# Performance work log

Measured on AMD Instinct MI355X. Metric: run time of the kernel, lower is better.

The kernel has to match this reference:

```python
import jax, jax.numpy as jnp
import numpy as np

GRID = 128          # fine voxel grid extent
N_PTS = 300000
C = 64              # hidden channels


def _encode(c, B):
    c = c.astype(np.int64)
    return (c[:, 0] * B + c[:, 1]) * B + c[:, 2]


def _kernel_map(in_coords, out_coords, offsets, n_out):
    """ME-style kernel map: for each kernel offset, (input_idx, output_idx) pairs
    where in_coord == out_coord + offset. Padded to a fixed length with a dummy
    output row n_out (sliced off later)."""
    B = GRID * 4
    keys = _encode(in_coords + 4, B)           # +4 shift keeps keys nonneg
    order = np.argsort(keys)
    skeys = keys[order]
    ins, outs = [], []
    for off in offsets:
        q = _encode(out_coords + 4 + off, B)
        pos = np.clip(np.searchsorted(skeys, q), 0, len(skeys) - 1)
        valid = skeys[pos] == q
        ins.append(order[pos[valid]].astype(np.int32))
        outs.append(np.nonzero(valid)[0].astype(np.int32))
    L = max(len(a) for a in ins)
    K = len(offsets)
    in_idx = np.zeros((K, L), np.int32)
    out_idx = np.full((K, L), n_out, np.int32)   # pad -> dummy row
    for k in range(K):
        m = len(ins[k])
        in_idx[k, :m] = ins[k]
        out_idx[k, :m] = outs[k]
    return in_idx, out_idx


def setup_inputs() -> dict:
    rng = np.random.default_rng(0)
    flat = rng.choice(GRID ** 3, size=N_PTS, replace=False)
    coords = np.stack(np.unravel_index(flat, (GRID,) * 3), axis=1).astype(np.int64)
    u = np.unique(coords // 2, axis=0)           # stride-2 output coords (coarse units)
    n2 = u.shape[0]

    r = np.arange(-1, 2)
    off27 = np.stack(np.meshgrid(r, r, r, indexing='ij'), -1).reshape(-1, 3)
    r2 = np.arange(0, 2)
    off8 = np.stack(np.meshgrid(r2, r2, r2, indexing='ij'), -1).reshape(-1, 3)

    map1_in, map1_out = _kernel_map(coords, coords, off27, N_PTS)   # k=3, s=1
    map2_in, map2_out = _kernel_map(coords, 2 * u, off8, n2)        # k=2, s=2
    map3_in, map3_out = _kernel_map(u, u, off27, n2)                # k=3, s=1 on coarse lattice

    key = jax.random.key(0)
    ks = jax.random.split(key, 8)
    sc1 = 1.0 / np.sqrt(27 * 8)
    sc2 = 1.0 / np.sqrt(8 * C)
    sc3 = 1.0 / np.sqrt(27 * C)
    return {
        'feats': jax.random.normal(ks[0], (N_PTS, 8), jnp.float32),
        'W1': jax.random.normal(ks[1], (27, 8, C), jnp.float32) * sc1,
        'b1': jax.random.normal(ks[2], (C,), jnp.float32) * 0.01,
        'W2': jax.random.normal(ks[3], (8, C, C), jnp.float32) * sc2,
        'b2': jax.random.normal(ks[4], (C,), jnp.float32) * 0.01,
        'W3': jax.random.normal(ks[5], (27, C, 8), jnp.float32) * sc3,
        'b3': jax.random.normal(ks[6], (8,), jnp.float32) * 0.01,
        'map1_in': jnp.asarray(map1_in), 'map1_out': jnp.asarray(map1_out),
        'map2_in': jnp.asarray(map2_in), 'map2_out': jnp.asarray(map2_out),
        'map3_in': jnp.asarray(map3_in), 'map3_out': jnp.asarray(map3_out),
        'n2': int(n2),
    }


def _sparse_conv(x, W, b, in_idx, out_idx, n_out):
    # gather-GEMM-scatter over K kernel offsets; padded pairs land on dummy row n_out
    y = jnp.zeros((n_out + 1, W.shape[-1]), x.dtype)
    for k in range(W.shape[0]):
        y = y.at[out_idx[k]].add(x[in_idx[k]] @ W[k])
    return y[:n_out] + b


def reference(feats, W1, b1, W2, b2, W3, b3,
              map1_in, map1_out, map2_in, map2_out, map3_in, map3_out, n2):
    n1 = feats.shape[0]
    h = jax.nn.relu(_sparse_conv(feats, W1, b1, map1_in, map1_out, n1))
    h = jax.nn.relu(_sparse_conv(h, W2, b2, map2_in, map2_out, n2))
    return _sparse_conv(h, W3, b3, map3_in, map3_out, n2)
```

## Files before the change

### kernel.cpp

```cpp
#include <hip/hip_runtime.h>


#define TPB 256

__device__ __forceinline__ int xcd_chunk(int bid, int nwg) {
  int q = nwg >> 3, r = nwg & 7;
  int xcd = bid & 7, idx = bid >> 3;
  int base = (xcd < r) ? xcd * (q + 1) : r * (q + 1) + (xcd - r) * q;
  return base + idx;
}

__global__ void __launch_bounds__(TPB)
k_build(const int* __restrict__ mi, const int* __restrict__ mo,
        int* __restrict__ tbl, int L, int n_out) {
  int k = blockIdx.y;
  int p = blockIdx.x * TPB + threadIdx.x;
  if (p >= L) return;
  int out = mo[(size_t)k * L + p];
  bool valid = out < n_out;
  if (__ballot(valid) == 0ull) return;
  if (valid) tbl[(size_t)k * n_out + out] = mi[(size_t)k * L + p];
}

__global__ void __launch_bounds__(TPB)
k_conv1(const float* __restrict__ x, const float* __restrict__ W1,
        const float* __restrict__ b1, const int* __restrict__ t1,
        float* __restrict__ h1, int n1) {
  int r = blockIdx.x * TPB + threadIdx.x;
  if (r >= n1) return;
  int j0 = blockIdx.y * 32;
  float acc[32];
#pragma unroll
  for (int j = 0; j < 32; ++j) acc[j] = 0.f;

  int icur = t1[r];
  const float4* xp = (const float4*)(x + (size_t)(icur >= 0 ? icur : 0) * 8);
  float4 ca = xp[0], cb = xp[1];
  bool vcur = icur >= 0;
#pragma unroll 1
  for (int k = 0; k < 27; ++k) {
    int inext = (k < 26) ? t1[(size_t)(k + 1) * n1 + r] : -1;
    const float4* np = (const float4*)(x + (size_t)(inext >= 0 ? inext : 0) * 8);
    float4 na = np[0], nb = np[1];
    if (!vcur) { ca = make_float4(0.f,0.f,0.f,0.f); cb = make_float4(0.f,0.f,0.f,0.f); }
    if (__ballot(vcur) != 0ull) {
      float xv[8] = {ca.x, ca.y, ca.z, ca.w, cb.x, cb.y, cb.z, cb.w};
      const float* __restrict__ Wk = W1 + (size_t)k * 512 + j0;
#pragma unroll
      for (int i = 0; i < 8; ++i)
#pragma unroll
        for (int j = 0; j < 32; ++j)
          acc[j] = fmaf(xv[i], Wk[i * 64 + j], acc[j]);
    }
    ca = na; cb = nb; vcur = inext >= 0;
  }
  float4* yr = (float4*)(h1 + (size_t)r * 64 + j0);
#pragma unroll
  for (int q = 0; q < 8; ++q) {
    float4 o;
    o.x = fmaxf(acc[4*q+0] + b1[j0+4*q+0], 0.f);
    o.y = fmaxf(acc[4*q+1] + b1[j0+4*q+1], 0.f);
    o.z = fmaxf(acc[4*q+2] + b1[j0+4*q+2], 0.f);
    o.w = fmaxf(acc[4*q+3] + b1[j0+4*q+3], 0.f);
    yr[q] = o;
  }
}

__global__ void __launch_bounds__(TPB)
k_conv2(const float* __restrict__ h1, const float* __restrict__ W2,
        const float* __restrict__ b2, const int* __restrict__ t2,
        float* __restrict__ h2, int n1, int n2, int nwg) {
  int b = xcd_chunk(blockIdx.x, nwg);
  int jq = b & 3, xb = b >> 2;
  int r = xb * TPB + threadIdx.x;
  if (r >= n2) return;
  int j0 = jq * 16;
  float acc[16];
#pragma unroll
  for (int j = 0; j < 16; ++j) acc[j] = 0.f;
  int idx = t2[r];
#pragma unroll 1
  for (int k = 0; k < 8; ++k) {
    int inext = (k < 7) ? t2[(size_t)(k + 1) * n2 + r] : 0;
    int row = idx >= 0 ? idx : n1;
    const float4* xr = (const float4*)(h1 + (size_t)row * 64);
    const float* __restrict__ Wk = W2 + (size_t)k * 4096 + j0;
#pragma unroll 4
    for (int c = 0; c < 16; ++c) {
      float4 xv = xr[c];
#pragma unroll
      for (int j = 0; j < 16; ++j) {
        acc[j] = fmaf(xv.x, Wk[(4*c+0)*64 + j], acc[j]);
        acc[j] = fmaf(xv.y, Wk[(4*c+1)*64 + j], acc[j]);
        acc[j] = fmaf(xv.z, Wk[(4*c+2)*64 + j], acc[j]);
        acc[j] = fmaf(xv.w, Wk[(4*c+3)*64 + j], acc[j]);
      }
    }
    idx = inext;
  }
  float4* yr = (float4*)(h2 + (size_t)r * 64 + j0);
#pragma unroll
  for (int q = 0; q < 4; ++q) {
    float4 o;
    o.x = fmaxf(acc[4*q+0] + b2[j0+4*q+0], 0.f);
    o.y = fmaxf(acc[4*q+1] + b2[j0+4*q+1], 0.f);
    o.z = fmaxf(acc[4*q+2] + b2[j0+4*q+2], 0.f);
    o.w = fmaxf(acc[4*q+3] + b2[j0+4*q+3], 0.f);
    yr[q] = o;
  }
}

__global__ void __launch_bounds__(TPB)
k_conv3(const float* __restrict__ h2, const float* __restrict__ W3,
        const float* __restrict__ b3, const int* __restrict__ t3,
        float* __restrict__ out, int n2, int nwg) {
  __shared__ float red[4][64][9];
  int b = xcd_chunk(blockIdx.x, nwg);
  int w = __builtin_amdgcn_readfirstlane(threadIdx.x >> 6);
  int l = threadIdx.x & 63;
  int r = b * 64 + l;
  int rc = r < n2 ? r : n2 - 1;
  float acc[8];
#pragma unroll
  for (int j = 0; j < 8; ++j) acc[j] = 0.f;
  int nk = (w < 3) ? 7 : 6;
  int idx = t3[(size_t)w * n2 + rc];
#pragma unroll 1
  for (int i = 0; i < nk; ++i) {
    int k = w + 4 * i;
    int row = idx >= 0 ? idx : n2;
    if (i + 1 < nk) idx = t3[(size_t)(k + 4) * n2 + rc];
    const float4* xr = (const float4*)(h2 + (size_t)row * 64);
    const float* __restrict__ Wk = W3 + (size_t)k * 512;
#pragma unroll
    for (int c = 0; c < 16; ++c) {
      float4 xv = xr[c];
      float hv[4] = {xv.x, xv.y, xv.z, xv.w};
#pragma unroll
      for (int u = 0; u < 4; ++u)
#pragma unroll
        for (int j = 0; j < 8; ++j)
          acc[j] = fmaf(hv[u], Wk[(4*c+u)*8 + j], acc[j]);
    }
  }
#pragma unroll
  for (int j = 0; j < 8; ++j) red[w][l][j] = acc[j];
  __syncthreads();
#pragma unroll
  for (int t = threadIdx.x; t < 512; t += TPB) {
    int row = t >> 3, ch = t & 7;
    int g = b * 64 + row;
    if (g < n2) {
      float s = red[0][row][ch] + red[1][row][ch]
              + red[2][row][ch] + red[3][row][ch];
      out[(size_t)g * 8 + ch] = s + b3[ch];
    }
  }
}

extern "C" void kernel_launch(void* const* d_in, const int* in_sizes, int n_in,
                              void* d_out, int out_size, void* d_ws, size_t ws_size,
                              hipStream_t stream) {
  const float* feats = (const float*)d_in[0];
  const float* W1 = (const float*)d_in[1];
  const float* b1 = (const float*)d_in[2];
  const float* W2 = (const float*)d_in[3];
  const float* b2 = (const float*)d_in[4];
  const float* W3 = (const float*)d_in[5];
  const float* b3 = (const float*)d_in[6];
  const int* m1i = (const int*)d_in[7];
  const int* m1o = (const int*)d_in[8];
  const int* m2i = (const int*)d_in[9];
  const int* m2o = (const int*)d_in[10];
  const int* m3i = (const int*)d_in[11];
  const int* m3o = (const int*)d_in[12];

  int n1 = in_sizes[0] / 8;
  int L1 = in_sizes[7] / 27;
  int L2 = in_sizes[9] / 8;
  int L3 = in_sizes[11] / 27;
  int n2 = out_size / 8;

  char* ws = (char*)d_ws;
  size_t y1_bytes = (size_t)(n1 + 1) * 64 * sizeof(float);
  size_t y2_bytes = (size_t)(n2 + 1) * 64 * sizeof(float);
  size_t t1_bytes = (size_t)27 * n1 * sizeof(int);
  size_t reg1_bytes = y2_bytes > t1_bytes ? y2_bytes : t1_bytes;
  float* y1 = (float*)ws;
  float* y2 = (float*)(ws + y1_bytes);
  int* t1 = (int*)(ws + y1_bytes);
  int* t2 = (int*)(ws + y1_bytes + reg1_bytes);
  int* t3 = (int*)(ws + y1_bytes + reg1_bytes + (size_t)8 * n2 * sizeof(int));

  hipMemsetAsync(t1, 0xFF, t1_bytes, stream);
  hipMemsetAsync(t2, 0xFF, (size_t)8 * n2 * sizeof(int), stream);
  hipMemsetAsync(t3, 0xFF, (size_t)27 * n2 * sizeof(int), stream);

  k_build<<<dim3((L1 + TPB - 1) / TPB, 27), TPB, 0, stream>>>(m1i, m1o, t1, L1, n1);
  k_build<<<dim3((L2 + TPB - 1) / TPB, 8), TPB, 0, stream>>>(m2i, m2o, t2, L2, n2);
  k_build<<<dim3((L3 + TPB - 1) / TPB, 27), TPB, 0, stream>>>(m3i, m3o, t3, L3, n2);

  k_conv1<<<dim3((n1 + TPB - 1) / TPB, 2), TPB, 0, stream>>>(feats, W1, b1, t1, y1, n1);

  hipMemsetAsync(y1 + (size_t)n1 * 64, 0, 64 * sizeof(float), stream);
  hipMemsetAsync(y2 + (size_t)n2 * 64, 0, 64 * sizeof(float), stream);

  int nb2 = ((n2 + TPB - 1) / TPB) * 4;
  k_conv2<<<nb2, TPB, 0, stream>>>(y1, W2, b2, t2, y2, n1, n2, nb2);

  int nb3 = (n2 + 63) / 64;
  k_conv3<<<nb3, TPB, 0, stream>>>(y2, W3, b3, t3, (float*)d_out, n2, nb3);
}
```

Baseline: 568.9 us.

## Coalesce conv1 stores via LDS staging, double rows per thread in conv3

conv1 now stages each block's 256x32 activated outputs in shared memory and writes them back as coalesced float4 rows. Before, each thread wrote its own strided 128-byte chunk. conv3 now processes two output rows per thread (128 rows per block), so each weight load is reused across two gathered inputs and half as many blocks are launched. The two index-table memsets are merged into one contiguous memset. The costs are extra LDS use and a barrier in conv1, plus more registers and fewer blocks in conv3.

```diff
diff --git a/kernel.cpp b/kernel.cpp
--- a/kernel.cpp
+++ b/kernel.cpp
@@ -26,20 +26,23 @@
 k_conv1(const float* __restrict__ x, const float* __restrict__ W1,
         const float* __restrict__ b1, const int* __restrict__ t1,
         float* __restrict__ h1, int n1) {
-  int r = blockIdx.x * TPB + threadIdx.x;
-  if (r >= n1) return;
+  __shared__ float st[256][33];
+  int tid = threadIdx.x;
+  int r0 = blockIdx.x * TPB;
+  int r = r0 + tid;
+  int rc = r < n1 ? r : n1 - 1;
   int j0 = blockIdx.y * 32;
   float acc[32];
 #pragma unroll
   for (int j = 0; j < 32; ++j) acc[j] = 0.f;
 
-  int icur = t1[r];
+  int icur = t1[rc];
   const float4* xp = (const float4*)(x + (size_t)(icur >= 0 ? icur : 0) * 8);
   float4 ca = xp[0], cb = xp[1];
   bool vcur = icur >= 0;
 #pragma unroll 1
   for (int k = 0; k < 27; ++k) {
-    int inext = (k < 26) ? t1[(size_t)(k + 1) * n1 + r] : -1;
+    int inext = (k < 26) ? t1[(size_t)(k + 1) * n1 + rc] : -1;
     const float4* np = (const float4*)(x + (size_t)(inext >= 0 ? inext : 0) * 8);
     float4 na = np[0], nb = np[1];
     if (!vcur) { ca = make_float4(0.f,0.f,0.f,0.f); cb = make_float4(0.f,0.f,0.f,0.f); }
@@ -54,15 +57,19 @@
     }
     ca = na; cb = nb; vcur = inext >= 0;
   }
-  float4* yr = (float4*)(h1 + (size_t)r * 64 + j0);
-#pragma unroll
-  for (int q = 0; q < 8; ++q) {
-    float4 o;
-    o.x = fmaxf(acc[4*q+0] + b1[j0+4*q+0], 0.f);
-    o.y = fmaxf(acc[4*q+1] + b1[j0+4*q+1], 0.f);
-    o.z = fmaxf(acc[4*q+2] + b1[j0+4*q+2], 0.f);
-    o.w = fmaxf(acc[4*q+3] + b1[j0+4*q+3], 0.f);
-    yr[q] = o;
+#pragma unroll
+  for (int j = 0; j < 32; ++j) st[tid][j] = fmaxf(acc[j] + b1[j0 + j], 0.f);
+  __syncthreads();
+#pragma unroll
+  for (int i = 0; i < 8; ++i) {
+    int f = i * 256 + tid;
+    int row = f >> 3, q = f & 7;
+    int g = r0 + row;
+    if (g < n1) {
+      float4 v = make_float4(st[row][4*q+0], st[row][4*q+1],
+                             st[row][4*q+2], st[row][4*q+3]);
+      *(float4*)(h1 + (size_t)g * 64 + j0 + 4 * q) = v;
+    }
   }
 }
 
@@ -114,42 +121,63 @@
 k_conv3(const float* __restrict__ h2, const float* __restrict__ W3,
         const float* __restrict__ b3, const int* __restrict__ t3,
         float* __restrict__ out, int n2, int nwg) {
-  __shared__ float red[4][64][9];
+  __shared__ float red[4][128][9];
   int b = xcd_chunk(blockIdx.x, nwg);
   int w = __builtin_amdgcn_readfirstlane(threadIdx.x >> 6);
   int l = threadIdx.x & 63;
-  int r = b * 64 + l;
-  int rc = r < n2 ? r : n2 - 1;
-  float acc[8];
-#pragma unroll
-  for (int j = 0; j < 8; ++j) acc[j] = 0.f;
+  int R = b * 128;
+  int rA = R + l, rB = R + 64 + l;
+  int rcA = rA < n2 ? rA : n2 - 1;
+  int rcB = rB < n2 ? rB : n2 - 1;
+  float accA[8], accB[8];
+#pragma unroll
+  for (int j = 0; j < 8; ++j) { accA[j] = 0.f; accB[j] = 0.f; }
   int nk = (w < 3) ? 7 : 6;
-  int idx = t3[(size_t)w * n2 + rc];
+  int idxA = t3[(size_t)w * n2 + rcA];
+  int idxB = t3[(size_t)w * n2 + rcB];
 #pragma unroll 1
   for (int i = 0; i < nk; ++i) {
     int k = w + 4 * i;
-    int row = idx >= 0 ? idx : n2;
-    if (i + 1 < nk) idx = t3[(size_t)(k + 4) * n2 + rc];
-    const float4* xr = (const float4*)(h2 + (size_t)row * 64);
+    int rowA = idxA >= 0 ? idxA : n2;
+    int rowB = idxB >= 0 ? idxB : n2;
+    if (i + 1 < nk) {
+      idxA = t3[(size_t)(k + 4) * n2 + rcA];
+      idxB = t3[(size_t)(k + 4) * n2 + rcB];
+    }
+    const float4* xrA = (const float4*)(h2 + (size_t)rowA * 64);
+    const float4* xrB = (const float4*)(h2 + (size_t)rowB * 64);
     const float* __restrict__ Wk = W3 + (size_t)k * 512;
 #pragma unroll
     for (int c = 0; c < 16; ++c) {
-      float4 xv = xr[c];
+      float4 xv = xrA[c];
       float hv[4] = {xv.x, xv.y, xv.z, xv.w};
 #pragma unroll
       for (int u = 0; u < 4; ++u)
 #pragma unroll
         for (int j = 0; j < 8; ++j)
-          acc[j] = fmaf(hv[u], Wk[(4*c+u)*8 + j], acc[j]);
-    }
-  }
-#pragma unroll
-  for (int j = 0; j < 8; ++j) red[w][l][j] = acc[j];
+          accA[j] = fmaf(hv[u], Wk[(4*c+u)*8 + j], accA[j]);
+    }
+#pragma unroll
+    for (int c = 0; c < 16; ++c) {
+      float4 xv = xrB[c];
+      float hv[4] = {xv.x, xv.y, xv.z, xv.w};
+#pragma unroll
+      for (int u = 0; u < 4; ++u)
+#pragma unroll
+        for (int j = 0; j < 8; ++j)
+          accB[j] = fmaf(hv[u], Wk[(4*c+u)*8 + j], accB[j]);
+    }
+  }
+#pragma unroll
+  for (int j = 0; j < 8; ++j) {
+    red[w][l][j] = accA[j];
+    red[w][64 + l][j] = accB[j];
+  }
   __syncthreads();
 #pragma unroll
-  for (int t = threadIdx.x; t < 512; t += TPB) {
+  for (int t = threadIdx.x; t < 1024; t += TPB) {
     int row = t >> 3, ch = t & 7;
-    int g = b * 64 + row;
+    int g = R + row;
     if (g < n2) {
       float s = red[0][row][ch] + red[1][row][ch]
               + red[2][row][ch] + red[3][row][ch];
@@ -193,8 +221,7 @@
   int* t3 = (int*)(ws + y1_bytes + reg1_bytes + (size_t)8 * n2 * sizeof(int));
 
   hipMemsetAsync(t1, 0xFF, t1_bytes, stream);
-  hipMemsetAsync(t2, 0xFF, (size_t)8 * n2 * sizeof(int), stream);
-  hipMemsetAsync(t3, 0xFF, (size_t)27 * n2 * sizeof(int), stream);
+  hipMemsetAsync(t2, 0xFF, (size_t)35 * n2 * sizeof(int), stream);
 
   k_build<<<dim3((L1 + TPB - 1) / TPB, 27), TPB, 0, stream>>>(m1i, m1o, t1, L1, n1);
   k_build<<<dim3((L2 + TPB - 1) / TPB, 8), TPB, 0, stream>>>(m2i, m2o, t2, L2, n2);
@@ -208,6 +235,6 @@
   int nb2 = ((n2 + TPB - 1) / TPB) * 4;
   k_conv2<<<nb2, TPB, 0, stream>>>(y1, W2, b2, t2, y2, n1, n2, nb2);
 
-  int nb3 = (n2 + 63) / 64;
+  int nb3 = (n2 + 127) / 128;
   k_conv3<<<nb3, TPB, 0, stream>>>(y2, W3, b3, t3, (float*)d_out, n2, nb3);
 }
```

New measurement: 587.3 us. +3.2%, slower.
